# Optimization experiments

Hardware: AMD Instinct MI355X
Metric: run time of the kernel (lower is better)

Reference implementation:

```python
import jax, jax.numpy as jnp
import numpy as np

# module config (from init_kwargs / hardcoded in module)
P = 0.075                      # pillar_size
H, W = 1440, 1440              # bev_spatial_shape(point_cloud_range, P)
GZ, VZ = 32, 0.25              # grid_size z, voxel_size z
GT, VT = 10, 0.05              # grid_size_t t, temp_size t
Z_CENTER = (8.0 + 0.0) / 2.0   # (pcr[5]+pcr[2])/2
T_ZCENTER = 5.0
N, B, C = 200_000, 2, 64


def setup_inputs() -> dict:
    key = jax.random.key(0)
    k1, k2 = jax.random.split(key, 2)
    u = jax.random.uniform(k1, (N, 5), dtype=jnp.float32)
    # cols: x,y in [0,108), z in [0,8), intensity in [0,1), t in [0,0.5)
    scale = jnp.array([108.0, 108.0, 8.0, 1.0, 0.5], dtype=jnp.float32) * 0.999
    xyzt = u * scale
    point_features = jax.random.normal(k2, (N, C), dtype=jnp.float32)
    xyz_batch_cnt = jnp.array([N // 2, N - N // 2], dtype=jnp.int32)
    return {"xyzt": xyzt, "xyz_batch_cnt": xyz_batch_cnt, "point_features": point_features}


def _batch_ids(cnt, n):
    # point -> batch id via prefix-sum search (stack-batched layout)
    return jnp.searchsorted(jnp.cumsum(cnt), jnp.arange(n), side="right").astype(jnp.int32)


def _unique_bins(flat, n):
    # sorted-unique of flat grid indices == cumsum-over-mask pillar ordering of the CUDA kernel
    FILL = jnp.int32(2**31 - 1)
    uniq, inv = jnp.unique(flat, size=n, fill_value=FILL, return_inverse=True)
    return uniq, inv.reshape(-1).astype(jnp.int32), uniq < FILL


def reference(xyzt, xyz_batch_cnt, point_features):
    n = xyzt.shape[0]
    b = _batch_ids(xyz_batch_cnt, n)
    xyz = xyzt[:, :3]
    xyt = xyzt[:, jnp.array([0, 1, 4])]
    x, y, z, t = xyzt[:, 0], xyzt[:, 1], xyzt[:, 2], xyzt[:, 4]
    ix = (x / P).astype(jnp.int32)
    iy = (y / P).astype(jnp.int32)
    iz = (z / VZ).astype(jnp.int32)
    it = (t / VT).astype(jnp.int32)

    # ---- 2D BEV pillars: gen_indice_pairs ----
    flat2 = (b * H + iy) * W + ix
    u2, inv2, v2 = _unique_bins(flat2, n)
    pb = u2 // (H * W)
    rem = u2 % (H * W)
    py, px = rem // W, rem % W
    points_coords = jnp.where(v2[:, None], jnp.stack([pb, py, px], axis=1), -1).astype(jnp.int32)
    f_center = jnp.stack([(px + 0.5) * P, (py + 0.5) * P, jnp.full_like(px, Z_CENTER, dtype=jnp.float32)], axis=1).astype(jnp.float32)

    # ---- 3D z voxels: gen_indice_pairs_3D with grid (1440,1440,32) ----
    flat3 = ((b * H + iy) * W + ix) * GZ + iz
    u3, inv3, v3 = _unique_bins(flat3, n)
    vb = u3 // (H * W * GZ)
    r = u3 % (H * W * GZ)
    vy = r // (W * GZ)
    r = r % (W * GZ)
    vx, vz = r // GZ, r % GZ
    # pillars layout [b,y,x,z]; output reordered [:, [0,3,1,2]] -> [b,z,y,x]
    points_coords_Z = jnp.where(v3[:, None], jnp.stack([vb, vz, vy, vx], axis=1), -1).astype(jnp.int32)
    z_center = jnp.stack([(vx + 0.5) * P, (vy + 0.5) * P, jnp.full_like(vx, Z_CENTER, dtype=jnp.float32)], axis=1).astype(jnp.float32)

    # ---- temporal voxels: gen_indice_pairs_3D on (x,y,t), grid (1440,1440,10), z_center=5 ----
    flatt = ((b * H + iy) * W + ix) * GT + it
    ut, invt, vt = _unique_bins(flatt, n)
    tb = ut // (H * W * GT)
    r = ut % (H * W * GT)
    ty = r // (W * GT)
    r = r % (W * GT)
    tx, tt = r // GT, r % GT
    points_coords_T = jnp.where(vt[:, None], jnp.stack([tb, tt, ty, tx], axis=1), -1).astype(jnp.int32)
    t_center = jnp.stack([(tx + 0.5) * P, (ty + 0.5) * P, jnp.full_like(tx, T_ZCENTER, dtype=jnp.float32)], axis=1).astype(jnp.float32)

    # ---- grouping: K=1 neighbor per point, all points in-range -> identity gather ----
    features = jnp.concatenate([point_features, xyz, xyz - f_center[inv2]], axis=1)
    z_features = jnp.concatenate([point_features, xyz, xyz - z_center[inv3]], axis=1)
    t_features = jnp.concatenate([point_features, xyt, xyt - t_center[invt]], axis=1)

    return (points_coords, inv2, features,
            points_coords_Z, inv3, z_features,
            points_coords_T, invt, t_features)
```

## Files before the change

### kernel.cpp

```cpp
#include <hip/hip_runtime.h>


namespace {
constexpr int   Hc  = 1440, Wc = 1440;
constexpr float Pf  = 0.075f, VZf = 0.25f, VTf = 0.05f;
constexpr int   GZi = 32, GTi = 10;
constexpr float ZCf = 4.0f, TZCf = 5.0f;

constexpr unsigned REGB_WORD  = 65024u;
constexpr unsigned REGC_WORD  = 2138624u;
constexpr unsigned TOT_WORDS  = 2786816u;
constexpr unsigned N_CHUNKS   = 10886u;
constexpr unsigned REGB_CHUNK = 254u;
constexpr unsigned REGC_CHUNK = 8354u;
}

__device__ __forceinline__ void compute_bins(const float* xyzt, int i, int cnt0,
    int& bb, int& ix, int& iy, int& iz, int& it,
    float& x, float& y, float& z, float& t) {
  const float* p = xyzt + (size_t)i * 5;
  x = p[0]; y = p[1]; z = p[2]; t = p[4];
  ix = (int)(x / Pf);  iy = (int)(y / Pf);
  iz = (int)(z / VZf); it = (int)(t / VTf);
  bb = (i >= cnt0) ? 1 : 0;
}

__global__ void fill_neg1_kernel(float4* out4, int n) {
  unsigned idx = blockIdx.x * blockDim.x + threadIdx.x;
  unsigned nq = (unsigned)n / 4u;
  unsigned cA = 3u * nq, cB = 4u * nq;
  unsigned tot = cA + 2u * cB;
  if (idx >= tot) return;
  size_t o;
  if (idx < cA)            o = idx;
  else if (idx < cA + cB)  o = (size_t)74 * nq + (idx - cA);
  else                     o = (size_t)149 * nq + (idx - cA - cB);
  out4[o] = make_float4(-1.f, -1.f, -1.f, -1.f);
}

__global__ void scatter_bits_kernel(const float* xyzt, const int* cnt, int n,
                                    unsigned long long* bitmap) {
  int i = blockIdx.x * blockDim.x + threadIdx.x;
  if (i >= n) return;
  int cnt0 = cnt[0];
  int bb, ix, iy, iz, it; float x, y, z, t;
  compute_bins(xyzt, i, cnt0, bb, ix, iy, iz, it, x, y, z, t);
  unsigned f2 = (unsigned)((bb * Hc + iy) * Wc + ix);
  unsigned f3 = f2 * (unsigned)GZi + (unsigned)iz;
  unsigned ft = f2 * (unsigned)GTi + (unsigned)it;
  atomicOr(&bitmap[f2 >> 6], 1ull << (f2 & 63));
  atomicOr(&bitmap[REGB_WORD + (f3 >> 6)], 1ull << (f3 & 63));
  atomicOr(&bitmap[REGC_WORD + (ft >> 6)], 1ull << (ft & 63));
}

__global__ __launch_bounds__(256) void scan1_kernel(
    const unsigned long long* bitmap, unsigned* wordPrefix, unsigned* chunkSums) {
  unsigned tid = threadIdx.x;
  unsigned lane = tid & 63u;
  unsigned chunk = blockIdx.x * 4u + (tid >> 6);
  if (chunk >= N_CHUNKS) return;
  unsigned wbase = chunk * 256u + lane * 4u;
  const ulonglong2* bp = (const ulonglong2*)(bitmap + wbase);
  ulonglong2 w01 = bp[0], w23 = bp[1];
  unsigned p0 = (unsigned)__popcll(w01.x), p1 = (unsigned)__popcll(w01.y);
  unsigned p2 = (unsigned)__popcll(w23.x), p3 = (unsigned)__popcll(w23.y);
  unsigned lsum = p0 + p1 + p2 + p3;
  unsigned x = lsum;
  #pragma unroll
  for (int d = 1; d < 64; d <<= 1) {
    unsigned o = __shfl_up(x, d, 64);
    if ((int)lane >= d) x += o;
  }
  unsigned excl = x - lsum;
  uint4 wp;
  wp.x = excl; wp.y = excl + p0; wp.z = excl + p0 + p1; wp.w = excl + p0 + p1 + p2;
  *(uint4*)(wordPrefix + wbase) = wp;
  if (lane == 63u) chunkSums[chunk] = x;
}

__global__ void scan2_kernel(const unsigned* chunkSums, unsigned* chunkPrefix) {
  __shared__ unsigned s[256];
  unsigned tid = threadIdx.x;
  const unsigned K = (N_CHUNKS + 255u) / 256u;
  unsigned base = tid * K;
  unsigned end = min(base + K, N_CHUNKS);
  unsigned sum = 0;
  for (unsigned j = base; j < end; ++j) sum += chunkSums[j];
  s[tid] = sum;
  __syncthreads();
  for (int o = 1; o < 256; o <<= 1) {
    unsigned v = (tid >= (unsigned)o) ? s[tid - o] : 0u;
    __syncthreads();
    s[tid] += v;
    __syncthreads();
  }
  unsigned run = s[tid] - sum;
  for (unsigned j = base; j < end; ++j) {
    unsigned v = chunkSums[j];
    chunkPrefix[j] = run;
    run += v;
  }
}

__global__ __launch_bounds__(256) void features_kernel(
    const float* xyzt, const float* pf, int n, float* out) {
  unsigned idx = blockIdx.x * blockDim.x + threadIdx.x;
  unsigned tot = 35u * (unsigned)n;
  if (idx >= tot) return;
  unsigned i = idx / 35u;
  unsigned c2 = idx - i * 35u;
  size_t nn = (size_t)n;
  float2* f  = (float2*)(out + 4 * nn);
  float2* zf = (float2*)(out + 79 * nn);
  float2* tf = (float2*)(out + 154 * nn);
  size_t r = (size_t)i * 35 + c2;
  float2 v, vt;
  if (c2 < 32u) {
    v = ((const float2*)pf)[(size_t)i * 32 + c2];
    vt = v;
  } else {
    const float* p = xyzt + (size_t)i * 5;
    float x = p[0], y = p[1], z = p[2], t = p[4];
    int ix = (int)(x / Pf), iy = (int)(y / Pf);
    float cx = ((float)ix + 0.5f) * Pf, cy = ((float)iy + 0.5f) * Pf;
    if (c2 == 32u)      { v = make_float2(x, y);        vt = v; }
    else if (c2 == 33u) { v = make_float2(z, x - cx);   vt = make_float2(t, x - cx); }
    else                { v = make_float2(y - cy, z - ZCf); vt = make_float2(y - cy, t - TZCf); }
  }
  f[r] = v; zf[r] = v; tf[r] = vt;
}

__global__ __launch_bounds__(256) void coords_kernel(
    const float* xyzt, const int* cnt, int n,
    const unsigned long long* bitmap, const unsigned* wordPrefix,
    const unsigned* chunkPrefix, float* out) {
  int i = blockIdx.x * blockDim.x + threadIdx.x;
  if (i >= n) return;
  int cnt0 = cnt[0];
  int bb, ix, iy, iz, it; float x, y, z, t;
  compute_bins(xyzt, i, cnt0, bb, ix, iy, iz, it, x, y, z, t);

  size_t nn = (size_t)n;
  const size_t o_coords  = 0,        o_inv2 = 3 * nn;
  const size_t o_coordsZ = 74 * nn,  o_inv3 = 78 * nn;
  const size_t o_coordsT = 149 * nn, o_invt = 153 * nn;

  unsigned f2 = (unsigned)((bb * Hc + iy) * Wc + ix);
  unsigned f3 = f2 * (unsigned)GZi + (unsigned)iz;
  unsigned ft = f2 * (unsigned)GTi + (unsigned)it;
  auto rank = [&](unsigned wordOff, unsigned vv) -> unsigned {
    unsigned w = wordOff + (vv >> 6);
    unsigned bit = vv & 63u;
    return chunkPrefix[w >> 8] + wordPrefix[w] +
           (unsigned)__popcll(bitmap[w] & ((1ull << bit) - 1ull));
  };
  unsigned r2 = rank(0u, f2);
  unsigned r3 = rank(REGB_WORD, f3) - chunkPrefix[REGB_CHUNK];
  unsigned rt = rank(REGC_WORD, ft) - chunkPrefix[REGC_CHUNK];
  out[o_inv2 + i] = (float)r2;
  out[o_inv3 + i] = (float)r3;
  out[o_invt + i] = (float)rt;
  float* pc2 = out + o_coords + (size_t)r2 * 3;
  pc2[0] = (float)bb; pc2[1] = (float)iy; pc2[2] = (float)ix;
  float* pz = out + o_coordsZ + (size_t)r3 * 4;
  pz[0] = (float)bb; pz[1] = (float)iz; pz[2] = (float)iy; pz[3] = (float)ix;
  float* pt = out + o_coordsT + (size_t)rt * 4;
  pt[0] = (float)bb; pt[1] = (float)it; pt[2] = (float)iy; pt[3] = (float)ix;
}

extern "C" void kernel_launch(void* const* d_in, const int* in_sizes, int n_in,
                              void* d_out, int out_size, void* d_ws, size_t ws_size,
                              hipStream_t stream) {
  const float* xyzt = (const float*)d_in[0];
  const int*   cnt  = (const int*)d_in[1];
  const float* pf   = (const float*)d_in[2];
  float* out = (float*)d_out;
  int n = in_sizes[0] / 5;

  unsigned long long* bitmap = (unsigned long long*)d_ws;
  unsigned* wordPrefix  = (unsigned*)((char*)d_ws + (size_t)TOT_WORDS * 8);
  unsigned* chunkSums   = (unsigned*)((char*)d_ws + (size_t)TOT_WORDS * 12);
  unsigned* chunkPrefix = chunkSums + ((N_CHUNKS + 7u) & ~7u);

  hipMemsetAsync(bitmap, 0, (size_t)TOT_WORDS * 8, stream);

  unsigned fillq = (unsigned)(11 * n / 4);
  fill_neg1_kernel<<<(fillq + 255) / 256, 256, 0, stream>>>((float4*)out, n);

  scatter_bits_kernel<<<(n + 255) / 256, 256, 0, stream>>>(xyzt, cnt, n, bitmap);

  scan1_kernel<<<(N_CHUNKS + 3) / 4, 256, 0, stream>>>(bitmap, wordPrefix, chunkSums);
  scan2_kernel<<<1, 256, 0, stream>>>(chunkSums, chunkPrefix);

  features_kernel<<<(35u * (unsigned)n + 255) / 256, 256, 0, stream>>>(xyzt, pf, n, out);

  coords_kernel<<<(n + 255) / 256, 256, 0, stream>>>(xyzt, cnt, n,
                                                     bitmap, wordPrefix, chunkPrefix, out);
}
```

Baseline: 305.5 us.

## Fuse bitmap scatter into features kernel and drop separate -1 fill pass

Folds the bitmap scatter into the features kernel, so one thread per point, the one handling the last float2 column, also issues the three atomicOr operations. The full -1 prefill kernel is removed. Instead the coords kernel writes -1 only to slots at or beyond the unique count, using a total that scan2 now appends after the chunk prefixes. Word prefixes shrink to 16-bit and scan2 runs with 1024 threads. This cuts two launches and the bulk fill writes, at the cost of atomics running inside a wide kernel with divergent lanes.

Result: faster. 283.8 us, median of 2 (-7.1%).

```diff
diff --git a/kernel.cpp b/kernel.cpp
--- a/kernel.cpp
+++ b/kernel.cpp
@@ -15,95 +15,9 @@
 constexpr unsigned REGC_CHUNK = 8354u;
 }
 
-__device__ __forceinline__ void compute_bins(const float* xyzt, int i, int cnt0,
-    int& bb, int& ix, int& iy, int& iz, int& it,
-    float& x, float& y, float& z, float& t) {
-  const float* p = xyzt + (size_t)i * 5;
-  x = p[0]; y = p[1]; z = p[2]; t = p[4];
-  ix = (int)(x / Pf);  iy = (int)(y / Pf);
-  iz = (int)(z / VZf); it = (int)(t / VTf);
-  bb = (i >= cnt0) ? 1 : 0;
-}
-
-__global__ void fill_neg1_kernel(float4* out4, int n) {
-  unsigned idx = blockIdx.x * blockDim.x + threadIdx.x;
-  unsigned nq = (unsigned)n / 4u;
-  unsigned cA = 3u * nq, cB = 4u * nq;
-  unsigned tot = cA + 2u * cB;
-  if (idx >= tot) return;
-  size_t o;
-  if (idx < cA)            o = idx;
-  else if (idx < cA + cB)  o = (size_t)74 * nq + (idx - cA);
-  else                     o = (size_t)149 * nq + (idx - cA - cB);
-  out4[o] = make_float4(-1.f, -1.f, -1.f, -1.f);
-}
-
-__global__ void scatter_bits_kernel(const float* xyzt, const int* cnt, int n,
-                                    unsigned long long* bitmap) {
-  int i = blockIdx.x * blockDim.x + threadIdx.x;
-  if (i >= n) return;
-  int cnt0 = cnt[0];
-  int bb, ix, iy, iz, it; float x, y, z, t;
-  compute_bins(xyzt, i, cnt0, bb, ix, iy, iz, it, x, y, z, t);
-  unsigned f2 = (unsigned)((bb * Hc + iy) * Wc + ix);
-  unsigned f3 = f2 * (unsigned)GZi + (unsigned)iz;
-  unsigned ft = f2 * (unsigned)GTi + (unsigned)it;
-  atomicOr(&bitmap[f2 >> 6], 1ull << (f2 & 63));
-  atomicOr(&bitmap[REGB_WORD + (f3 >> 6)], 1ull << (f3 & 63));
-  atomicOr(&bitmap[REGC_WORD + (ft >> 6)], 1ull << (ft & 63));
-}
-
-__global__ __launch_bounds__(256) void scan1_kernel(
-    const unsigned long long* bitmap, unsigned* wordPrefix, unsigned* chunkSums) {
-  unsigned tid = threadIdx.x;
-  unsigned lane = tid & 63u;
-  unsigned chunk = blockIdx.x * 4u + (tid >> 6);
-  if (chunk >= N_CHUNKS) return;
-  unsigned wbase = chunk * 256u + lane * 4u;
-  const ulonglong2* bp = (const ulonglong2*)(bitmap + wbase);
-  ulonglong2 w01 = bp[0], w23 = bp[1];
-  unsigned p0 = (unsigned)__popcll(w01.x), p1 = (unsigned)__popcll(w01.y);
-  unsigned p2 = (unsigned)__popcll(w23.x), p3 = (unsigned)__popcll(w23.y);
-  unsigned lsum = p0 + p1 + p2 + p3;
-  unsigned x = lsum;
-  #pragma unroll
-  for (int d = 1; d < 64; d <<= 1) {
-    unsigned o = __shfl_up(x, d, 64);
-    if ((int)lane >= d) x += o;
-  }
-  unsigned excl = x - lsum;
-  uint4 wp;
-  wp.x = excl; wp.y = excl + p0; wp.z = excl + p0 + p1; wp.w = excl + p0 + p1 + p2;
-  *(uint4*)(wordPrefix + wbase) = wp;
-  if (lane == 63u) chunkSums[chunk] = x;
-}
-
-__global__ void scan2_kernel(const unsigned* chunkSums, unsigned* chunkPrefix) {
-  __shared__ unsigned s[256];
-  unsigned tid = threadIdx.x;
-  const unsigned K = (N_CHUNKS + 255u) / 256u;
-  unsigned base = tid * K;
-  unsigned end = min(base + K, N_CHUNKS);
-  unsigned sum = 0;
-  for (unsigned j = base; j < end; ++j) sum += chunkSums[j];
-  s[tid] = sum;
-  __syncthreads();
-  for (int o = 1; o < 256; o <<= 1) {
-    unsigned v = (tid >= (unsigned)o) ? s[tid - o] : 0u;
-    __syncthreads();
-    s[tid] += v;
-    __syncthreads();
-  }
-  unsigned run = s[tid] - sum;
-  for (unsigned j = base; j < end; ++j) {
-    unsigned v = chunkSums[j];
-    chunkPrefix[j] = run;
-    run += v;
-  }
-}
-
-__global__ __launch_bounds__(256) void features_kernel(
-    const float* xyzt, const float* pf, int n, float* out) {
+__global__ __launch_bounds__(256) void features_scatter_kernel(
+    const float* xyzt, const float* pf, const int* cnt, int n,
+    unsigned long long* bitmap, float* out) {
   unsigned idx = blockIdx.x * blockDim.x + threadIdx.x;
   unsigned tot = 35u * (unsigned)n;
   if (idx >= tot) return;
@@ -125,25 +39,97 @@
     float cx = ((float)ix + 0.5f) * Pf, cy = ((float)iy + 0.5f) * Pf;
     if (c2 == 32u)      { v = make_float2(x, y);        vt = v; }
     else if (c2 == 33u) { v = make_float2(z, x - cx);   vt = make_float2(t, x - cx); }
-    else                { v = make_float2(y - cy, z - ZCf); vt = make_float2(y - cy, t - TZCf); }
+    else {
+      v = make_float2(y - cy, z - ZCf); vt = make_float2(y - cy, t - TZCf);
+      int bb = (i >= (unsigned)cnt[0]) ? 1 : 0;
+      int iz = (int)(z / VZf), it = (int)(t / VTf);
+      unsigned f2 = (unsigned)((bb * Hc + iy) * Wc + ix);
+      unsigned f3 = f2 * (unsigned)GZi + (unsigned)iz;
+      unsigned ft = f2 * (unsigned)GTi + (unsigned)it;
+      atomicOr(&bitmap[f2 >> 6], 1ull << (f2 & 63));
+      atomicOr(&bitmap[REGB_WORD + (f3 >> 6)], 1ull << (f3 & 63));
+      atomicOr(&bitmap[REGC_WORD + (ft >> 6)], 1ull << (ft & 63));
+    }
   }
   f[r] = v; zf[r] = v; tf[r] = vt;
 }
 
+__global__ __launch_bounds__(256) void scan1_kernel(
+    const unsigned long long* bitmap, unsigned short* wordPrefix, unsigned* chunkSums) {
+  unsigned tid = threadIdx.x;
+  unsigned lane = tid & 63u;
+  unsigned chunk = blockIdx.x * 4u + (tid >> 6);
+  if (chunk >= N_CHUNKS) return;
+  unsigned wbase = chunk * 256u + lane * 4u;
+  const ulonglong2* bp = (const ulonglong2*)(bitmap + wbase);
+  ulonglong2 w01 = bp[0], w23 = bp[1];
+  unsigned p0 = (unsigned)__popcll(w01.x), p1 = (unsigned)__popcll(w01.y);
+  unsigned p2 = (unsigned)__popcll(w23.x), p3 = (unsigned)__popcll(w23.y);
+  unsigned lsum = p0 + p1 + p2 + p3;
+  unsigned x = lsum;
+  #pragma unroll
+  for (int d = 1; d < 64; d <<= 1) {
+    unsigned o = __shfl_up(x, d, 64);
+    if ((int)lane >= d) x += o;
+  }
+  unsigned excl = x - lsum;
+  ushort4 wp;
+  wp.x = (unsigned short)excl;
+  wp.y = (unsigned short)(excl + p0);
+  wp.z = (unsigned short)(excl + p0 + p1);
+  wp.w = (unsigned short)(excl + p0 + p1 + p2);
+  *(ushort4*)(wordPrefix + wbase) = wp;
+  if (lane == 63u) chunkSums[chunk] = x;
+}
+
+__global__ __launch_bounds__(1024) void scan2_kernel(
+    const unsigned* chunkSums, unsigned* chunkPrefix) {
+  __shared__ unsigned s[1024];
+  unsigned tid = threadIdx.x;
+  const unsigned K = (N_CHUNKS + 1023u) / 1024u;
+  unsigned base = tid * K;
+  unsigned end = min(base + K, N_CHUNKS);
+  unsigned sum = 0;
+  for (unsigned j = base; j < end; ++j) sum += chunkSums[j];
+  s[tid] = sum;
+  __syncthreads();
+  for (int o = 1; o < 1024; o <<= 1) {
+    unsigned v = (tid >= (unsigned)o) ? s[tid - o] : 0u;
+    __syncthreads();
+    s[tid] += v;
+    __syncthreads();
+  }
+  unsigned run = s[tid] - sum;
+  for (unsigned j = base; j < end; ++j) {
+    unsigned v = chunkSums[j];
+    chunkPrefix[j] = run;
+    run += v;
+  }
+  if (tid == 1023u) chunkPrefix[N_CHUNKS] = s[1023];
+}
+
 __global__ __launch_bounds__(256) void coords_kernel(
     const float* xyzt, const int* cnt, int n,
-    const unsigned long long* bitmap, const unsigned* wordPrefix,
+    const unsigned long long* bitmap, const unsigned short* wordPrefix,
     const unsigned* chunkPrefix, float* out) {
   int i = blockIdx.x * blockDim.x + threadIdx.x;
   if (i >= n) return;
   int cnt0 = cnt[0];
-  int bb, ix, iy, iz, it; float x, y, z, t;
-  compute_bins(xyzt, i, cnt0, bb, ix, iy, iz, it, x, y, z, t);
+  const float* p = xyzt + (size_t)i * 5;
+  float x = p[0], y = p[1], z = p[2], t = p[4];
+  int ix = (int)(x / Pf), iy = (int)(y / Pf);
+  int iz = (int)(z / VZf), it = (int)(t / VTf);
+  int bb = (i >= cnt0) ? 1 : 0;
 
   size_t nn = (size_t)n;
   const size_t o_coords  = 0,        o_inv2 = 3 * nn;
   const size_t o_coordsZ = 74 * nn,  o_inv3 = 78 * nn;
   const size_t o_coordsT = 149 * nn, o_invt = 153 * nn;
+
+  unsigned cumA = chunkPrefix[REGB_CHUNK];
+  unsigned cumB = chunkPrefix[REGC_CHUNK];
+  unsigned cumT = chunkPrefix[N_CHUNKS];
+  unsigned uniqA = cumA, uniqZ = cumB - cumA, uniqT = cumT - cumB;
 
   unsigned f2 = (unsigned)((bb * Hc + iy) * Wc + ix);
   unsigned f3 = f2 * (unsigned)GZi + (unsigned)iz;
@@ -151,12 +137,12 @@
   auto rank = [&](unsigned wordOff, unsigned vv) -> unsigned {
     unsigned w = wordOff + (vv >> 6);
     unsigned bit = vv & 63u;
-    return chunkPrefix[w >> 8] + wordPrefix[w] +
+    return chunkPrefix[w >> 8] + (unsigned)wordPrefix[w] +
            (unsigned)__popcll(bitmap[w] & ((1ull << bit) - 1ull));
   };
   unsigned r2 = rank(0u, f2);
-  unsigned r3 = rank(REGB_WORD, f3) - chunkPrefix[REGB_CHUNK];
-  unsigned rt = rank(REGC_WORD, ft) - chunkPrefix[REGC_CHUNK];
+  unsigned r3 = rank(REGB_WORD, f3) - cumA;
+  unsigned rt = rank(REGC_WORD, ft) - cumB;
   out[o_inv2 + i] = (float)r2;
   out[o_inv3 + i] = (float)r3;
   out[o_invt + i] = (float)rt;
@@ -166,6 +152,19 @@
   pz[0] = (float)bb; pz[1] = (float)iz; pz[2] = (float)iy; pz[3] = (float)ix;
   float* pt = out + o_coordsT + (size_t)rt * 4;
   pt[0] = (float)bb; pt[1] = (float)it; pt[2] = (float)iy; pt[3] = (float)ix;
+
+  if ((unsigned)i >= uniqA) {
+    float* q = out + o_coords + (size_t)i * 3;
+    q[0] = -1.f; q[1] = -1.f; q[2] = -1.f;
+  }
+  if ((unsigned)i >= uniqZ) {
+    float4* q = (float4*)(out + o_coordsZ) + i;
+    *q = make_float4(-1.f, -1.f, -1.f, -1.f);
+  }
+  if ((unsigned)i >= uniqT) {
+    float* qs = out + o_coordsT + (size_t)i * 4;
+    qs[0] = -1.f; qs[1] = -1.f; qs[2] = -1.f; qs[3] = -1.f;
+  }
 }
 
 extern "C" void kernel_launch(void* const* d_in, const int* in_sizes, int n_in,
@@ -178,21 +177,17 @@
   int n = in_sizes[0] / 5;
 
   unsigned long long* bitmap = (unsigned long long*)d_ws;
-  unsigned* wordPrefix  = (unsigned*)((char*)d_ws + (size_t)TOT_WORDS * 8);
-  unsigned* chunkSums   = (unsigned*)((char*)d_ws + (size_t)TOT_WORDS * 12);
+  unsigned short* wordPrefix = (unsigned short*)((char*)d_ws + (size_t)TOT_WORDS * 8);
+  unsigned* chunkSums   = (unsigned*)((char*)d_ws + (size_t)TOT_WORDS * 10);
   unsigned* chunkPrefix = chunkSums + ((N_CHUNKS + 7u) & ~7u);
 
   hipMemsetAsync(bitmap, 0, (size_t)TOT_WORDS * 8, stream);
 
-  unsigned fillq = (unsigned)(11 * n / 4);
-  fill_neg1_kernel<<<(fillq + 255) / 256, 256, 0, stream>>>((float4*)out, n);
-
-  scatter_bits_kernel<<<(n + 255) / 256, 256, 0, stream>>>(xyzt, cnt, n, bitmap);
+  features_scatter_kernel<<<(35u * (unsigned)n + 255) / 256, 256, 0, stream>>>(
+      xyzt, pf, cnt, n, bitmap, out);
 
   scan1_kernel<<<(N_CHUNKS + 3) / 4, 256, 0, stream>>>(bitmap, wordPrefix, chunkSums);
-  scan2_kernel<<<1, 256, 0, stream>>>(chunkSums, chunkPrefix);
-
-  features_kernel<<<(35u * (unsigned)n + 255) / 256, 256, 0, stream>>>(xyzt, pf, n, out);
+  scan2_kernel<<<1, 1024, 0, stream>>>(chunkSums, chunkPrefix);
 
   coords_kernel<<<(n + 255) / 256, 256, 0, stream>>>(xyzt, cnt, n,
                                                      bitmap, wordPrefix, chunkPrefix, out);
```
